# Optimization experiments

Hardware: AMD Instinct MI355X
Metric: run time of the kernel (lower is better)

Reference implementation:

```python
import jax, jax.numpy as jnp
import numpy as np

H, D, C, K, N, B = 16, 64, 1024, 256, 4096, 2

def setup_inputs() -> dict:
    key = jax.random.key(0)
    ks = jax.random.split(key, 10)
    s = lambda k, shp, fan: jax.random.normal(k, shp, jnp.float32) * (1.0 / np.sqrt(fan))
    return {
        "x": jax.random.normal(ks[0], (B, N, C), jnp.float32),
        "Wq": s(ks[1], (H, D, C), C),   # per-head Linear(channels->dim), no bias
        "Wk": s(ks[2], (H, D, C), C),
        "Wv": s(ks[3], (H, D, C), C),
        "We": s(ks[4], (H, K, N), N),   # E: Linear(input_size->dim_k)
        "bE": jnp.zeros((H, K), jnp.float32),
        "Wf": s(ks[5], (H, K, N), N),   # F: Linear(input_size->dim_k)
        "bF": jnp.zeros((H, K), jnp.float32),
        "Wo": s(ks[6], (C, H * D), H * D),
        "bo": jnp.zeros((C,), jnp.float32),
    }

def reference(x, Wq, Wk, Wv, We, bE, Wf, bF, Wo, bo):
    b, n, c = x.shape
    h, d = Wq.shape[0], Wq.shape[1]
    # per-head Q/K/V projections, vectorized over heads: [b,h,n,d]
    Q = jnp.einsum('bnc,hdc->bhnd', x, Wq)
    Kt = jnp.einsum('bnc,hdc->bhdn', x, Wk)   # K already transposed(1,2)
    Vt = jnp.einsum('bnc,hdc->bhdn', x, Wv)   # V transposed(1,2)
    # Linformer E/F low-rank projections along sequence axis -> [b,h,d,k]
    Ke = jnp.einsum('bhdn,hkn->bhdk', Kt, We) + bE[None, :, None, :]
    Vf = jnp.einsum('bhdn,hkn->bhdk', Vt, Wf) + bF[None, :, None, :]
    # scaled scores + softmax over low-rank dim k
    scores = jnp.einsum('bhnd,bhdk->bhnk', Q, Kt if False else Ke) / jnp.sqrt(jnp.asarray(d, x.dtype))
    P = jax.nn.softmax(scores, axis=-1)
    # P @ V_f^T  -> [b,h,n,d]
    out = jnp.einsum('bhnk,bhkd->bhnd', P, jnp.swapaxes(Vf, -1, -2))
    # concat heads -> [b,n,h*d]
    out = jnp.transpose(out, (0, 2, 1, 3)).reshape(b, n, h * d)
    out = jax.nn.gelu(out, approximate=False)
    return out @ Wo.T + bo
```

## Files before the change

### kernel.cpp

```cpp
#include <hip/hip_runtime.h>

typedef unsigned short u16;
typedef float f32x4 __attribute__((ext_vector_type(4)));
typedef short s16x8 __attribute__((ext_vector_type(8)));
typedef unsigned short u16x4 __attribute__((ext_vector_type(4)));

__device__ __forceinline__ u16 f2bf(float f) {
  union { float f; unsigned u; } v; v.f = f;
  unsigned r = v.u + 0x7FFFu + ((v.u >> 16) & 1u);
  return (u16)(r >> 16);
}

__device__ __forceinline__ void gload_lds16(const void* g, void* l) {
  __builtin_amdgcn_global_load_lds(
      (const __attribute__((address_space(1))) void*)g,
      (__attribute__((address_space(3))) void*)l, 16, 0, 0);
}

__global__ __launch_bounds__(256) void cast_f32_bf16(
    const float* __restrict__ src, u16* __restrict__ dst, int n4) {
  int i = blockIdx.x * 256 + threadIdx.x;
  if (i >= n4) return;
  f32x4 v = ((const f32x4*)src)[i];
  u16x4 o = { f2bf(v[0]), f2bf(v[1]), f2bf(v[2]), f2bf(v[3]) };
  ((u16x4*)dst)[i] = o;
}

template <int MODE>
__global__ __launch_bounds__(256, 2) void gemm_pipe(
    const u16* __restrict__ A, const u16* __restrict__ B,
    void* __restrict__ Cout, const float* __restrict__ bias,
    u16* __restrict__ KT, u16* __restrict__ VT,
    int K, int lda, int ldb, int ldc) {
  __shared__ char smem[3 * 8192 + 3 * 16384];
  const int tid = threadIdx.x;
  const int wid = tid >> 6, lane = tid & 63;
  const int lo = lane & 15, hi = lane >> 4;
  const int wr = wid >> 1, wc = wid & 1;
  const long brow = (long)blockIdx.y * 128;
  const long bcol = (long)blockIdx.x * 256;
  const int T = K >> 5;

  f32x4 acc[4][8] = {};

  const char* Ab = (const char*)(A + (size_t)brow * lda);
  const char* Bb = (const char*)(B + (size_t)bcol * ldb);
  const size_t ldab = (size_t)lda * 2, ldbb = (size_t)ldb * 2;

  const int LA0 = wid * 2048 + lane * 16, LA1 = LA0 + 1024;
  const int LB0 = wid * 4096 + lane * 16, LB1 = LB0 + 1024;
  const int LB2 = LB0 + 2048, LB3 = LB0 + 3072;
#define SRCCOL(L) (((L) & 63) ^ ((((L) >> 7) & 3) << 4))
  const char* aS0 = Ab + (size_t)(LA0 >> 6) * ldab + SRCCOL(LA0);
  const char* aS1 = Ab + (size_t)(LA1 >> 6) * ldab + SRCCOL(LA1);
  const char* bS0 = Bb + (size_t)(LB0 >> 6) * ldbb + SRCCOL(LB0);
  const char* bS1 = Bb + (size_t)(LB1 >> 6) * ldbb + SRCCOL(LB1);
  const char* bS2 = Bb + (size_t)(LB2 >> 6) * ldbb + SRCCOL(LB2);
  const char* bS3 = Bb + (size_t)(LB3 >> 6) * ldbb + SRCCOL(LB3);
#undef SRCCOL

  int ra[4], rb[8];
#pragma unroll
  for (int m = 0; m < 4; ++m) {
    int row = wr * 64 + m * 16 + lo;
    ra[m] = row * 64 + ((hi ^ ((row >> 1) & 3)) << 4);
  }
#pragma unroll
  for (int n = 0; n < 8; ++n) {
    int row = wc * 128 + n * 16 + lo;
    rb[n] = row * 64 + ((hi ^ ((row >> 1) & 3)) << 4);
  }

#define STAGE(t)                                                    \
  {                                                                 \
    char* sa_ = smem + ((t) % 3) * 8192;                            \
    char* sb_ = smem + 24576 + ((t) % 3) * 16384;                   \
    size_t kb_ = (size_t)(t) << 6;                                  \
    gload_lds16(aS0 + kb_, sa_ + LA0);                              \
    gload_lds16(aS1 + kb_, sa_ + LA1);                              \
    gload_lds16(bS0 + kb_, sb_ + LB0);                              \
    gload_lds16(bS1 + kb_, sb_ + LB1);                              \
    gload_lds16(bS2 + kb_, sb_ + LB2);                              \
    gload_lds16(bS3 + kb_, sb_ + LB3);                              \
  }

  STAGE(0); STAGE(1);
  asm volatile("s_waitcnt vmcnt(6)" ::: "memory");
  __builtin_amdgcn_s_barrier();
  __builtin_amdgcn_sched_barrier(0);

  for (int t = 0; t < T; ++t) {
    const char* sa = smem + (t % 3) * 8192;
    const char* sb = smem + 24576 + (t % 3) * 16384;
    s16x8 af[4], bf[8];
#pragma unroll
    for (int m = 0; m < 4; ++m) af[m] = *(const s16x8*)(sa + ra[m]);
#pragma unroll
    for (int n = 0; n < 8; ++n) bf[n] = *(const s16x8*)(sb + rb[n]);
    if (t + 2 < T) STAGE(t + 2);
    __builtin_amdgcn_s_setprio(1);
#pragma unroll
    for (int m = 0; m < 4; ++m)
#pragma unroll
      for (int n = 0; n < 8; ++n)
        acc[m][n] = __builtin_amdgcn_mfma_f32_16x16x32_bf16(af[m], bf[n], acc[m][n], 0, 0, 0);
    __builtin_amdgcn_s_setprio(0);
    if (t + 2 < T) asm volatile("s_waitcnt vmcnt(6)" ::: "memory");
    else           asm volatile("s_waitcnt vmcnt(0)" ::: "memory");
    __builtin_amdgcn_s_barrier();
    __builtin_amdgcn_sched_barrier(0);
  }
#undef STAGE

  if (MODE == 1) {
#pragma unroll
    for (int m = 0; m < 4; ++m)
#pragma unroll
      for (int n = 0; n < 8; ++n)
#pragma unroll
        for (int r = 0; r < 4; ++r) {
          size_t row = brow + wr * 64 + m * 16 + hi * 4 + r;
          size_t col = bcol + wc * 128 + n * 16 + lo;
          ((float*)Cout)[row * ldc + col] = acc[m][n][r] + bias[col];
        }
  } else {
    const int kind = (int)(bcol >> 10);
    if (kind == 0) {
#pragma unroll
      for (int m = 0; m < 4; ++m)
#pragma unroll
        for (int n = 0; n < 8; ++n)
#pragma unroll
          for (int r = 0; r < 4; ++r) {
            size_t row = brow + wr * 64 + m * 16 + hi * 4 + r;
            size_t col = bcol + wc * 128 + n * 16 + lo;
            ((u16*)Cout)[row * 1024 + col] = f2bf(acc[m][n][r]);
          }
    } else {
      u16* Tp = (kind == 1) ? KT : VT;
#pragma unroll
      for (int m = 0; m < 4; ++m)
#pragma unroll
        for (int n = 0; n < 8; ++n) {
          int col = (int)(bcol + wc * 128 + n * 16 + lo);
          int lc = col & 1023, h = lc >> 6, d = lc & 63;
          size_t n0 = brow + wr * 64 + m * 16 + hi * 4;
          int b = (int)(n0 >> 12), nin = (int)(n0 & 4095);
          u16x4 w = { f2bf(acc[m][n][0]), f2bf(acc[m][n][1]),
                      f2bf(acc[m][n][2]), f2bf(acc[m][n][3]) };
          *(u16x4*)(Tp + (((size_t)b * 16 + h) * 64 + d) * 4096 + nin) = w;
        }
    }
  }
}

__global__ __launch_bounds__(256) void kevf_kernel(
    const float* __restrict__ We, const float* __restrict__ Wf,
    const u16* __restrict__ KT, const u16* __restrict__ VT,
    float* __restrict__ part) {
  __shared__ u16 As[2][64 * 64];
  __shared__ u16 Bs[3][64 * 64];
  const int type = blockIdx.z >> 2, ns = blockIdx.z & 3;
  const int bh = blockIdx.y, h = bh & 15;
  const int kk0 = blockIdx.x * 64;
  const float* W = (type ? Wf : We) + ((size_t)(h * 256 + kk0)) * 4096;
  const u16* T = (type ? VT : KT) + (size_t)bh * 64 * 4096;
  const int tid = threadIdx.x, wid = tid >> 6, lane = tid & 63;
  const int lo = lane & 15, hi = lane >> 4;
  const int nbeg = ns << 10;

  const int wrow = tid >> 2;
  const float* wsrc = W + (size_t)wrow * 4096 + nbeg + (tid & 3) * 16;
  const int aw0 = wrow * 128 + (((tid & 3) * 32) ^ ((wrow & 7) << 4));
  const int aw1 = wrow * 128 + (((tid & 3) * 32 + 16) ^ ((wrow & 7) << 4));
  const int L0 = tid * 16, L1 = 4096 + tid * 16;
  const int tr0 = L0 >> 7, tc0 = (L0 & 127) ^ ((tr0 & 7) << 4);
  const int tr1 = L1 >> 7, tc1 = (L1 & 127) ^ ((tr1 & 7) << 4);
  const char* tS0 = (const char*)(T + (size_t)tr0 * 4096 + nbeg) + tc0;
  const char* tS1 = (const char*)(T + (size_t)tr1 * 4096 + nbeg) + tc1;

  const int dd = wid * 16 + lo;
  const int raK0 = dd * 128 + ((hi * 16) ^ ((dd & 7) << 4));
  const int raK1 = dd * 128 + ((64 + hi * 16) ^ ((dd & 7) << 4));
  int rbW[4][2];
#pragma unroll
  for (int dt = 0; dt < 4; ++dt) {
    int r = dt * 16 + lo;
    rbW[dt][0] = r * 128 + ((hi * 16) ^ ((r & 7) << 4));
    rbW[dt][1] = r * 128 + ((64 + hi * 16) ^ ((r & 7) << 4));
  }

  f32x4 acc[4] = {};
  f32x4 Aw0, Aw1, Aw2, Aw3, Bw0, Bw1, Bw2, Bw3;

#define WISSUE(S, t) { const float* p_ = wsrc + (size_t)(t) * 64;  \
    S##w0 = *(const f32x4*)p_;       S##w1 = *(const f32x4*)(p_ + 4); \
    S##w2 = *(const f32x4*)(p_ + 8); S##w3 = *(const f32x4*)(p_ + 12); }
#define TISSUE(t) { size_t kb_ = (size_t)(t) * 128;                \
    gload_lds16(tS0 + kb_, (char*)Bs[(t) % 3] + L0);               \
    gload_lds16(tS1 + kb_, (char*)Bs[(t) % 3] + L1); }

#define KSTEP(S, t) {                                                     \
    if ((t) < 14) asm volatile("s_waitcnt vmcnt(6)" ::: "memory");        \
    else          asm volatile("s_waitcnt vmcnt(0)" ::: "memory");        \
    s16x8 w0_, w1_;                                                       \
    _Pragma("unroll")                                                     \
    for (int j = 0; j < 4; ++j) {                                         \
      w0_[j]     = (short)f2bf(S##w0[j]); w0_[j + 4] = (short)f2bf(S##w1[j]); \
      w1_[j]     = (short)f2bf(S##w2[j]); w1_[j + 4] = (short)f2bf(S##w3[j]); \
    }                                                                     \
    *(s16x8*)((char*)As[(t) & 1] + aw0) = w0_;                            \
    *(s16x8*)((char*)As[(t) & 1] + aw1) = w1_;                            \
    asm volatile("s_waitcnt lgkmcnt(0)" ::: "memory");                    \
    __builtin_amdgcn_s_barrier();                                         \
    __builtin_amdgcn_sched_barrier(0);                                    \
    const char* bs_ = (const char*)Bs[(t) % 3];                           \
    const char* as_ = (const char*)As[(t) & 1];                           \
    s16x8 a0_ = *(const s16x8*)(bs_ + raK0);                              \
    s16x8 a1_ = *(const s16x8*)(bs_ + raK1);                              \
    s16x8 bfr_[4][2];                                                     \
    _Pragma("unroll")                                                     \
    for (int dt = 0; dt < 4; ++dt) {                                      \
      bfr_[dt][0] = *(const s16x8*)(as_ + rbW[dt][0]);                    \
      bfr_[dt][1] = *(const s16x8*)(as_ + rbW[dt][1]);                    \
    }                                                                     \
    if ((t) + 2 < 16) { WISSUE(S, (t) + 2); TISSUE((t) + 2); }            \
    __builtin_amdgcn_s_setprio(1);                                        \
    _Pragma("unroll")                                                     \
    for (int dt = 0; dt < 4; ++dt) {                                      \
      acc[dt] = __builtin_amdgcn_mfma_f32_16x16x32_bf16(a0_, bfr_[dt][0], acc[dt], 0, 0, 0); \
      acc[dt] = __builtin_amdgcn_mfma_f32_16x16x32_bf16(a1_, bfr_[dt][1], acc[dt], 0, 0, 0); \
    }                                                                     \
    __builtin_amdgcn_s_setprio(0);                                        \
    __builtin_amdgcn_s_barrier();                                         \
    __builtin_amdgcn_sched_barrier(0);                                    \
  }

  WISSUE(A, 0); TISSUE(0); WISSUE(B, 1); TISSUE(1);
  KSTEP(A, 0);  KSTEP(B, 1);  KSTEP(A, 2);  KSTEP(B, 3);
  KSTEP(A, 4);  KSTEP(B, 5);  KSTEP(A, 6);  KSTEP(B, 7);
  KSTEP(A, 8);  KSTEP(B, 9);  KSTEP(A, 10); KSTEP(B, 11);
  KSTEP(A, 12); KSTEP(B, 13); KSTEP(A, 14); KSTEP(B, 15);
#undef WISSUE
#undef TISSUE
#undef KSTEP

  const size_t pbase = ((size_t)((type * 32 + bh) * 4 + blockIdx.x) * 4 + ns) * 4096;
#pragma unroll
  for (int dt = 0; dt < 4; ++dt)
#pragma unroll
    for (int r = 0; r < 4; ++r)
      part[pbase + (size_t)(wid * 16 + hi * 4 + r) * 64 + dt * 16 + lo] = acc[dt][r];
}

__global__ __launch_bounds__(256) void kevf_reduce(
    const float* __restrict__ part, const float* __restrict__ bE,
    const float* __restrict__ bF, u16* __restrict__ KeT, u16* __restrict__ Vf) {
  const int tb = blockIdx.x;
  const int type = tb >> 7, bh = (tb >> 2) & 31, kc = tb & 3;
  const int t = threadIdx.x;
  const int dd = t >> 2, kkc = (t & 3) * 16;
  const float* p = part + (size_t)tb * 16384 + dd * 64 + kkc;
  f32x4 s[4];
#pragma unroll
  for (int j = 0; j < 4; ++j) s[j] = ((const f32x4*)p)[j];
#pragma unroll
  for (int ns = 1; ns < 4; ++ns)
#pragma unroll
    for (int j = 0; j < 4; ++j) {
      f32x4 v = ((const f32x4*)(p + ns * 4096))[j];
      s[j][0] += v[0]; s[j][1] += v[1]; s[j][2] += v[2]; s[j][3] += v[3];
    }
  const int h = bh & 15;
  const float* bv = (type ? bF : bE) + h * 256 + kc * 64 + kkc;
  if (type == 0) {
#pragma unroll
    for (int j = 0; j < 4; ++j)
#pragma unroll
      for (int e = 0; e < 4; ++e) {
        int kk = kkc + j * 4 + e;
        KeT[((size_t)bh * 256 + kc * 64 + kk) * 64 + dd] = f2bf(s[j][e] + bv[j * 4 + e]);
      }
  } else {
    u16* o = Vf + ((size_t)bh * 64 + dd) * 256 + kc * 64 + kkc;
#pragma unroll
    for (int j = 0; j < 4; ++j) {
      u16x4 w = { f2bf(s[j][0] + bv[j * 4 + 0]), f2bf(s[j][1] + bv[j * 4 + 1]),
                  f2bf(s[j][2] + bv[j * 4 + 2]), f2bf(s[j][3] + bv[j * 4 + 3]) };
      *(u16x4*)(o + j * 4) = w;
    }
  }
}

__global__ __launch_bounds__(256) void attn_fused(
    const u16* __restrict__ Q, const u16* __restrict__ KeT,
    const u16* __restrict__ Vf, u16* __restrict__ attn) {
  __shared__ char smem[65536];
  char* sKe = smem;
  char* sVf = smem + 32768;
  const int tid = threadIdx.x, wid = tid >> 6, lane = tid & 63;
  const int lo = lane & 15, hi = lane >> 4;
  const int bh = blockIdx.y, b = bh >> 4, h = bh & 15;
  const int n0 = blockIdx.x * 64;

  const char* keg = (const char*)(KeT + (size_t)bh * 256 * 64);
  const char* vfg = (const char*)(Vf + (size_t)bh * 64 * 256);
#pragma unroll
  for (int i = 0; i < 8; ++i) {
    int ob = wid * 8192 + i * 1024;
    int o = ob + lane * 16;
    int kr = o >> 7, kc = o & 127;
    gload_lds16(keg + kr * 128 + (kc ^ ((kr & 7) << 4)), sKe + ob);
    int vr = o >> 9, vc = o & 511;
    gload_lds16(vfg + vr * 512 + (vc ^ ((vr & 7) << 4)), sVf + ob);
  }
  const u16* qp = Q + (size_t)(b * 4096 + n0 + wid * 16 + lo) * 1024 + h * 64;
  s16x8 qf0 = *(const s16x8*)(qp + hi * 8);
  s16x8 qf1 = *(const s16x8*)(qp + 32 + hi * 8);
  __syncthreads();

  f32x4 sc[16];
#pragma unroll
  for (int nt = 0; nt < 16; ++nt) {
    int kk = nt * 16 + lo;
    int sw = (kk & 7) << 4;
    s16x8 b0 = *(const s16x8*)(sKe + kk * 128 + ((hi * 16) ^ sw));
    s16x8 b1 = *(const s16x8*)(sKe + kk * 128 + ((64 + hi * 16) ^ sw));
    f32x4 c = {0.f, 0.f, 0.f, 0.f};
    c = __builtin_amdgcn_mfma_f32_16x16x32_bf16(qf0, b0, c, 0, 0, 0);
    c = __builtin_amdgcn_mfma_f32_16x16x32_bf16(qf1, b1, c, 0, 0, 0);
    sc[nt] = c;
  }
  float mx[4], inv[4];
#pragma unroll
  for (int r = 0; r < 4; ++r) {
    float m = sc[0][r];
#pragma unroll
    for (int nt = 1; nt < 16; ++nt) m = fmaxf(m, sc[nt][r]);
    m = fmaxf(m, __shfl_xor(m, 1));
    m = fmaxf(m, __shfl_xor(m, 2));
    m = fmaxf(m, __shfl_xor(m, 4));
    m = fmaxf(m, __shfl_xor(m, 8));
    mx[r] = m;
  }
  const float SCL = 0.125f * 1.4426950408889634f;
  float sm[4] = {0.f, 0.f, 0.f, 0.f};
#pragma unroll
  for (int nt = 0; nt < 16; ++nt)
#pragma unroll
    for (int r = 0; r < 4; ++r) {
      float p = exp2f((sc[nt][r] - mx[r]) * SCL);
      sc[nt][r] = p;
      sm[r] += p;
    }
#pragma unroll
  for (int r = 0; r < 4; ++r) {
    float s = sm[r];
    s += __shfl_xor(s, 1);
    s += __shfl_xor(s, 2);
    s += __shfl_xor(s, 4);
    s += __shfl_xor(s, 8);
    inv[r] = 1.0f / s;
  }
  __syncthreads();
  char* pb = smem + wid * 8192;
#pragma unroll
  for (int nt = 0; nt < 16; ++nt)
#pragma unroll
    for (int r = 0; r < 4; ++r) {
      int row = hi * 4 + r;
      int kk = nt * 16 + lo;
      *(u16*)(pb + row * 512 + ((kk * 2) ^ ((row & 7) << 4))) = f2bf(sc[nt][r] * inv[r]);
    }
  __syncthreads();
  s16x8 pa[8];
#pragma unroll
  for (int ks = 0; ks < 8; ++ks)
    pa[ks] = *(const s16x8*)(pb + lo * 512 + ((ks * 64 + hi * 16) ^ ((lo & 7) << 4)));
#pragma unroll
  for (int dt = 0; dt < 4; ++dt) {
    int dd = dt * 16 + lo;
    int sw = (dd & 7) << 4;
    f32x4 o = {0.f, 0.f, 0.f, 0.f};
#pragma unroll
    for (int ks = 0; ks < 8; ++ks) {
      s16x8 vb = *(const s16x8*)(sVf + dd * 512 + ((ks * 64 + hi * 16) ^ sw));
      o = __builtin_amdgcn_mfma_f32_16x16x32_bf16(pa[ks], vb, o, 0, 0, 0);
    }
#pragma unroll
    for (int r = 0; r < 4; ++r) {
      int row = n0 + wid * 16 + hi * 4 + r;
      float x = o[r];
      float g = 0.5f * x * (1.0f + erff(x * 0.7071067811865476f));
      attn[(size_t)(b * 4096 + row) * 1024 + h * 64 + dd] = f2bf(g);
    }
  }
}

extern "C" void kernel_launch(void* const* d_in, const int* in_sizes, int n_in,
                              void* d_out, int out_size, void* d_ws, size_t ws_size,
                              hipStream_t stream) {
  const float* x  = (const float*)d_in[0];
  const float* Wq = (const float*)d_in[1];
  const float* Wk = (const float*)d_in[2];
  const float* Wv = (const float*)d_in[3];
  const float* We = (const float*)d_in[4];
  const float* bE = (const float*)d_in[5];
  const float* Wf = (const float*)d_in[6];
  const float* bF = (const float*)d_in[7];
  const float* Wo = (const float*)d_in[8];
  const float* bo = (const float*)d_in[9];
  float* out = (float*)d_out;

  char* ws = (char*)d_ws;
  u16* xb   = (u16*)(ws);
  u16* Wqkv = (u16*)(ws + 16777216);
  u16* Wob  = (u16*)(ws + 23068672);
  u16* Q    = (u16*)(ws + 25165824);
  u16* KT   = (u16*)(ws + 41943040);
  u16* VT   = (u16*)(ws + 58720256);
  u16* KeT  = (u16*)(ws + 75497472);
  u16* Vf   = (u16*)(ws + 76546048);
  u16* attn = (u16*)(ws + 77594624);
  float* part = (float*)(ws);

  cast_f32_bf16<<<8192, 256, 0, stream>>>(x, xb, 2097152);
  cast_f32_bf16<<<1024, 256, 0, stream>>>(Wq, Wqkv, 262144);
  cast_f32_bf16<<<1024, 256, 0, stream>>>(Wk, Wqkv + 1048576, 262144);
  cast_f32_bf16<<<1024, 256, 0, stream>>>(Wv, Wqkv + 2097152, 262144);
  cast_f32_bf16<<<1024, 256, 0, stream>>>(Wo, Wob, 262144);

  gemm_pipe<0><<<dim3(12, 64), 256, 0, stream>>>(xb, Wqkv, Q, nullptr, KT, VT,
                                                 1024, 1024, 1024, 1024);
  kevf_kernel<<<dim3(4, 32, 8), 256, 0, stream>>>(We, Wf, KT, VT, part);
  kevf_reduce<<<256, 256, 0, stream>>>(part, bE, bF, KeT, Vf);
  attn_fused<<<dim3(64, 32), 256, 0, stream>>>(Q, KeT, Vf, attn);
  gemm_pipe<1><<<dim3(4, 64), 256, 0, stream>>>(attn, Wob, out, bo, nullptr, nullptr,
                                                1024, 1024, 1024, 1024);
}
```

Baseline: 201.2 us.

## Split GEMM K-step into two half-tile phases interleaving loads and MFMAs

The main GEMM loop is split into two phases per K-step. Each phase loads half of the B fragments from LDS, issues half of the global-to-LDS prefetch for step t+2, and then runs half of the MFMAs. The goal is to spread memory issue across the compute so the LDS reads and global loads overlap better with the matrix cores. In exchange, each iteration now has several extra workgroup barriers and lgkmcnt waits, which can add synchronisation stalls.

```diff
diff --git a/kernel.cpp b/kernel.cpp
--- a/kernel.cpp
+++ b/kernel.cpp
@@ -71,7 +71,7 @@
     rb[n] = row * 64 + ((hi ^ ((row >> 1) & 3)) << 4);
   }
 
-#define STAGE(t)                                                    \
+#define STAGE_H1(t)                                                 \
   {                                                                 \
     char* sa_ = smem + ((t) % 3) * 8192;                            \
     char* sb_ = smem + 24576 + ((t) % 3) * 16384;                   \
@@ -79,12 +79,17 @@
     gload_lds16(aS0 + kb_, sa_ + LA0);                              \
     gload_lds16(aS1 + kb_, sa_ + LA1);                              \
     gload_lds16(bS0 + kb_, sb_ + LB0);                              \
+  }
+#define STAGE_H2(t)                                                 \
+  {                                                                 \
+    char* sb_ = smem + 24576 + ((t) % 3) * 16384;                   \
+    size_t kb_ = (size_t)(t) << 6;                                  \
     gload_lds16(bS1 + kb_, sb_ + LB1);                              \
     gload_lds16(bS2 + kb_, sb_ + LB2);                              \
     gload_lds16(bS3 + kb_, sb_ + LB3);                              \
   }
 
-  STAGE(0); STAGE(1);
+  STAGE_H1(0); STAGE_H2(0); STAGE_H1(1); STAGE_H2(1);
   asm volatile("s_waitcnt vmcnt(6)" ::: "memory");
   __builtin_amdgcn_s_barrier();
   __builtin_amdgcn_sched_barrier(0);
@@ -96,21 +101,38 @@
 #pragma unroll
     for (int m = 0; m < 4; ++m) af[m] = *(const s16x8*)(sa + ra[m]);
 #pragma unroll
-    for (int n = 0; n < 8; ++n) bf[n] = *(const s16x8*)(sb + rb[n]);
-    if (t + 2 < T) STAGE(t + 2);
+    for (int n = 0; n < 4; ++n) bf[n] = *(const s16x8*)(sb + rb[n]);
+    if (t + 2 < T) STAGE_H1(t + 2);
+    __builtin_amdgcn_s_barrier();
+    asm volatile("s_waitcnt lgkmcnt(0)" ::: "memory");
+    __builtin_amdgcn_sched_barrier(0);
     __builtin_amdgcn_s_setprio(1);
 #pragma unroll
     for (int m = 0; m < 4; ++m)
 #pragma unroll
-      for (int n = 0; n < 8; ++n)
+      for (int n = 0; n < 4; ++n)
         acc[m][n] = __builtin_amdgcn_mfma_f32_16x16x32_bf16(af[m], bf[n], acc[m][n], 0, 0, 0);
     __builtin_amdgcn_s_setprio(0);
+    __builtin_amdgcn_s_barrier();
+#pragma unroll
+    for (int n = 4; n < 8; ++n) bf[n] = *(const s16x8*)(sb + rb[n]);
+    if (t + 2 < T) STAGE_H2(t + 2);
     if (t + 2 < T) asm volatile("s_waitcnt vmcnt(6)" ::: "memory");
     else           asm volatile("s_waitcnt vmcnt(0)" ::: "memory");
     __builtin_amdgcn_s_barrier();
+    asm volatile("s_waitcnt lgkmcnt(0)" ::: "memory");
     __builtin_amdgcn_sched_barrier(0);
-  }
-#undef STAGE
+    __builtin_amdgcn_s_setprio(1);
+#pragma unroll
+    for (int m = 0; m < 4; ++m)
+#pragma unroll
+      for (int n = 4; n < 8; ++n)
+        acc[m][n] = __builtin_amdgcn_mfma_f32_16x16x32_bf16(af[m], bf[n], acc[m][n], 0, 0, 0);
+    __builtin_amdgcn_s_setprio(0);
+    __builtin_amdgcn_s_barrier();
+  }
+#undef STAGE_H1
+#undef STAGE_H2
 
   if (MODE == 1) {
 #pragma unroll
```

After: 202.5 us. About the same (+0.7%).

## Use 256x256-tile 8-wave QKV GEMM with 4-stage LDS pipeline and block swizzle

Applied to the files above, without the earlier changes.

Replaces the templated 128x256 QKV projection GEMM with a dedicated 512-thread kernel computing 256x256 tiles. It uses a 4-buffer LDS ring with 3 stages in flight, XOR-swizzled LDS layout, split A/B load phases interleaved with MFMA halves, and a remapped block index for L2 locality. The output GEMM becomes a separate non-templated kernel with the same logic. The goal is more reuse per loaded tile and better latency hiding in the largest GEMM. The cost is 128KB of LDS per block, which limits occupancy.

```diff
diff --git a/kernel.cpp b/kernel.cpp
--- a/kernel.cpp
+++ b/kernel.cpp
@@ -26,11 +26,127 @@
   ((u16x4*)dst)[i] = o;
 }
 
-template <int MODE>
-__global__ __launch_bounds__(256, 2) void gemm_pipe(
+__global__ __launch_bounds__(512, 2) void gemm256_qkv(
     const u16* __restrict__ A, const u16* __restrict__ B,
-    void* __restrict__ Cout, const float* __restrict__ bias,
-    u16* __restrict__ KT, u16* __restrict__ VT,
+    u16* __restrict__ Q, u16* __restrict__ KT, u16* __restrict__ VT,
+    int K, int lda, int ldb) {
+  __shared__ char smem[4 * 32768];
+  const int tid = threadIdx.x;
+  const int wid = tid >> 6, lane = tid & 63;
+  const int lo = lane & 15, hi = lane >> 4;
+  const int wm = wid >> 2, wn = wid & 3;
+  const int id = blockIdx.x + blockIdx.y * 12;
+  const int nid = (id & 7) * 48 + (id >> 3);
+  const long bcol = (long)(nid % 12) * 256;
+  const long brow = (long)(nid / 12) * 256;
+  const int T = K >> 5;
+
+  f32x4 acc[8][4] = {};
+
+  const size_t ldab = (size_t)lda * 2, ldbb = (size_t)ldb * 2;
+  const int rowS = wid * 32 + (lane >> 2);
+  const int colSwz = (((lane & 3) ^ ((lane >> 3) & 3)) << 4);
+  const char* aS0 = (const char*)A + (size_t)(brow + rowS) * ldab + colSwz;
+  const char* aS1 = aS0 + 16 * ldab;
+  const char* bS0 = (const char*)B + (size_t)(bcol + rowS) * ldbb + colSwz;
+  const char* bS1 = bS0 + 16 * ldbb;
+  const int dA0 = wid * 2048 + lane * 16, dA1 = dA0 + 1024;
+  const int dB0 = 16384 + dA0, dB1 = dB0 + 1024;
+
+  const int ksw = (hi ^ ((lo >> 1) & 3)) << 4;
+  int rdA[8], rdB[4];
+#pragma unroll
+  for (int mf = 0; mf < 8; ++mf) rdA[mf] = (wm * 128 + mf * 16 + lo) * 64 + ksw;
+#pragma unroll
+  for (int nf = 0; nf < 4; ++nf) rdB[nf] = 16384 + (wn * 64 + nf * 16 + lo) * 64 + ksw;
+
+#pragma unroll
+  for (int t = 0; t < 3; ++t) {
+    char* wb = smem + t * 32768;
+    size_t kb = (size_t)t * 64;
+    gload_lds16(aS0 + kb, wb + dA0);
+    gload_lds16(aS1 + kb, wb + dA1);
+    gload_lds16(bS0 + kb, wb + dB0);
+    gload_lds16(bS1 + kb, wb + dB1);
+  }
+  asm volatile("s_waitcnt vmcnt(8)" ::: "memory");
+  __builtin_amdgcn_s_barrier();
+  __builtin_amdgcn_sched_barrier(0);
+
+  for (int t = 0; t < T; ++t) {
+    const char* rb = smem + (t & 3) * 32768;
+    char* wb = smem + ((t + 3) & 3) * 32768;
+    const size_t kb = (size_t)(t + 3) * 64;
+    const bool st = (t + 3) < T;
+    s16x8 bfr[4], af[4];
+#pragma unroll
+    for (int nf = 0; nf < 4; ++nf) bfr[nf] = *(const s16x8*)(rb + rdB[nf]);
+#pragma unroll
+    for (int mf = 0; mf < 4; ++mf) af[mf] = *(const s16x8*)(rb + rdA[mf]);
+    if (st) { gload_lds16(aS0 + kb, wb + dA0); gload_lds16(aS1 + kb, wb + dA1); }
+    __builtin_amdgcn_s_barrier();
+    asm volatile("s_waitcnt lgkmcnt(0)" ::: "memory");
+    __builtin_amdgcn_sched_barrier(0);
+    __builtin_amdgcn_s_setprio(1);
+#pragma unroll
+    for (int mf = 0; mf < 4; ++mf)
+#pragma unroll
+      for (int nf = 0; nf < 4; ++nf)
+        acc[mf][nf] = __builtin_amdgcn_mfma_f32_16x16x32_bf16(af[mf], bfr[nf], acc[mf][nf], 0, 0, 0);
+    __builtin_amdgcn_s_setprio(0);
+    __builtin_amdgcn_s_barrier();
+#pragma unroll
+    for (int mf = 0; mf < 4; ++mf) af[mf] = *(const s16x8*)(rb + rdA[4 + mf]);
+    if (st) { gload_lds16(bS0 + kb, wb + dB0); gload_lds16(bS1 + kb, wb + dB1); }
+    __builtin_amdgcn_s_barrier();
+    asm volatile("s_waitcnt lgkmcnt(0)" ::: "memory");
+    __builtin_amdgcn_sched_barrier(0);
+    __builtin_amdgcn_s_setprio(1);
+#pragma unroll
+    for (int mf = 0; mf < 4; ++mf)
+#pragma unroll
+      for (int nf = 0; nf < 4; ++nf)
+        acc[4 + mf][nf] = __builtin_amdgcn_mfma_f32_16x16x32_bf16(af[mf], bfr[nf], acc[4 + mf][nf], 0, 0, 0);
+    __builtin_amdgcn_s_setprio(0);
+    if (t + 3 < T)      asm volatile("s_waitcnt vmcnt(8)" ::: "memory");
+    else if (t + 2 < T) asm volatile("s_waitcnt vmcnt(4)" ::: "memory");
+    else if (t + 1 < T) asm volatile("s_waitcnt vmcnt(0)" ::: "memory");
+    __builtin_amdgcn_s_barrier();
+    __builtin_amdgcn_sched_barrier(0);
+  }
+
+  const int kind = (int)(bcol >> 10);
+  if (kind == 0) {
+#pragma unroll
+    for (int mf = 0; mf < 8; ++mf)
+#pragma unroll
+      for (int nf = 0; nf < 4; ++nf)
+#pragma unroll
+        for (int r = 0; r < 4; ++r) {
+          size_t row = brow + wm * 128 + mf * 16 + hi * 4 + r;
+          size_t col = bcol + wn * 64 + nf * 16 + lo;
+          Q[row * 1024 + col] = f2bf(acc[mf][nf][r]);
+        }
+  } else {
+    u16* Tp = (kind == 1) ? KT : VT;
+#pragma unroll
+    for (int mf = 0; mf < 8; ++mf)
+#pragma unroll
+      for (int nf = 0; nf < 4; ++nf) {
+        int col = (int)(bcol + wn * 64 + nf * 16 + lo);
+        int lc = col & 1023, h = lc >> 6, d = lc & 63;
+        size_t n0 = brow + wm * 128 + mf * 16 + hi * 4;
+        int b = (int)(n0 >> 12), nin = (int)(n0 & 4095);
+        u16x4 w = { f2bf(acc[mf][nf][0]), f2bf(acc[mf][nf][1]),
+                    f2bf(acc[mf][nf][2]), f2bf(acc[mf][nf][3]) };
+        *(u16x4*)(Tp + (((size_t)b * 16 + h) * 64 + d) * 4096 + nin) = w;
+      }
+  }
+}
+
+__global__ __launch_bounds__(256, 2) void gemm_out(
+    const u16* __restrict__ A, const u16* __restrict__ B,
+    float* __restrict__ Cout, const float* __restrict__ bias,
     int K, int lda, int ldb, int ldc) {
   __shared__ char smem[3 * 8192 + 3 * 16384];
   const int tid = threadIdx.x;
@@ -112,46 +228,16 @@
   }
 #undef STAGE
 
-  if (MODE == 1) {
-#pragma unroll
-    for (int m = 0; m < 4; ++m)
-#pragma unroll
-      for (int n = 0; n < 8; ++n)
-#pragma unroll
-        for (int r = 0; r < 4; ++r) {
-          size_t row = brow + wr * 64 + m * 16 + hi * 4 + r;
-          size_t col = bcol + wc * 128 + n * 16 + lo;
-          ((float*)Cout)[row * ldc + col] = acc[m][n][r] + bias[col];
-        }
-  } else {
-    const int kind = (int)(bcol >> 10);
-    if (kind == 0) {
-#pragma unroll
-      for (int m = 0; m < 4; ++m)
-#pragma unroll
-        for (int n = 0; n < 8; ++n)
-#pragma unroll
-          for (int r = 0; r < 4; ++r) {
-            size_t row = brow + wr * 64 + m * 16 + hi * 4 + r;
-            size_t col = bcol + wc * 128 + n * 16 + lo;
-            ((u16*)Cout)[row * 1024 + col] = f2bf(acc[m][n][r]);
-          }
-    } else {
-      u16* Tp = (kind == 1) ? KT : VT;
-#pragma unroll
-      for (int m = 0; m < 4; ++m)
-#pragma unroll
-        for (int n = 0; n < 8; ++n) {
-          int col = (int)(bcol + wc * 128 + n * 16 + lo);
-          int lc = col & 1023, h = lc >> 6, d = lc & 63;
-          size_t n0 = brow + wr * 64 + m * 16 + hi * 4;
-          int b = (int)(n0 >> 12), nin = (int)(n0 & 4095);
-          u16x4 w = { f2bf(acc[m][n][0]), f2bf(acc[m][n][1]),
-                      f2bf(acc[m][n][2]), f2bf(acc[m][n][3]) };
-          *(u16x4*)(Tp + (((size_t)b * 16 + h) * 64 + d) * 4096 + nin) = w;
-        }
-    }
-  }
+#pragma unroll
+  for (int m = 0; m < 4; ++m)
+#pragma unroll
+    for (int n = 0; n < 8; ++n)
+#pragma unroll
+      for (int r = 0; r < 4; ++r) {
+        size_t row = brow + wr * 64 + m * 16 + hi * 4 + r;
+        size_t col = bcol + wc * 128 + n * 16 + lo;
+        Cout[row * ldc + col] = acc[m][n][r] + bias[col];
+      }
 }
 
 __global__ __launch_bounds__(256) void kevf_kernel(
@@ -430,11 +516,11 @@
   cast_f32_bf16<<<1024, 256, 0, stream>>>(Wv, Wqkv + 2097152, 262144);
   cast_f32_bf16<<<1024, 256, 0, stream>>>(Wo, Wob, 262144);
 
-  gemm_pipe<0><<<dim3(12, 64), 256, 0, stream>>>(xb, Wqkv, Q, nullptr, KT, VT,
-                                                 1024, 1024, 1024, 1024);
+  gemm256_qkv<<<dim3(12, 32), 512, 0, stream>>>(xb, Wqkv, Q, KT, VT,
+                                                1024, 1024, 1024);
   kevf_kernel<<<dim3(4, 32, 8), 256, 0, stream>>>(We, Wf, KT, VT, part);
   kevf_reduce<<<256, 256, 0, stream>>>(part, bE, bF, KeT, Vf);
   attn_fused<<<dim3(64, 32), 256, 0, stream>>>(Q, KeT, Vf, attn);
-  gemm_pipe<1><<<dim3(4, 64), 256, 0, stream>>>(attn, Wob, out, bo, nullptr, nullptr,
-                                                1024, 1024, 1024, 1024);
-}
+  gemm_out<<<dim3(4, 64), 256, 0, stream>>>(attn, Wob, out, bo,
+                                            1024, 1024, 1024, 1024);
+}
```

After: 209.8 us. 1.04x slower.
